# Kernel tuning notes

Measured on AMD Instinct MI355X. Metric: run time of the kernel, lower is better.

Reference implementation:

```python
import jax, jax.numpy as jnp
import numpy as np


def setup_inputs() -> dict:
    key = jax.random.key(0)
    B, N, D = 8, 2048, 512
    put = jax.random.normal(key, (B, N, D), dtype=jnp.float32)
    return {"put": put, "k": 16}


def reference(put, k):
    # put: [B, N, D]; k: python int
    B, N, _ = put.shape
    # squared-norm expansion of pairwise Euclidean distance
    xx = jnp.sum(put * put, axis=2, keepdims=True)            # [B, N, 1]
    gram = jnp.einsum('bnd,bmd->bnm', put, put)               # [B, N, N]
    dist2 = xx + jnp.swapaxes(xx, 1, 2) - 2.0 * gram          # [B, N, N]
    dist = jnp.sqrt(jnp.clip(dist2, 0.0))                     # clamp(min=0).sqrt()

    # k nearest (smallest distance): top_k of negated distances
    _, inc = jax.lax.top_k(-dist, k)                          # [B, N, k] int32

    # binary adjacency: out[b, j, inc[b, j, :]] = 1 (vectorized scatter)
    b_idx = jnp.arange(B)[:, None, None]                      # [B,1,1]
    r_idx = jnp.arange(N)[None, :, None]                      # [1,N,1]
    out = jnp.zeros_like(dist).at[b_idx, r_idx, inc].set(1.0)
    return out
```

## Files before the change

kernel.cpp:

```cpp
#include <hip/hip_runtime.h>
#include <cstdint>

#define NN 2048
#define DD 512
#define NB 8

using ull = unsigned long long;
typedef __attribute__((ext_vector_type(8))) short bf16x8;
typedef __attribute__((ext_vector_type(4))) float f32x4;

#define GLOAD_LDS16(g, l)                                                      \
  __builtin_amdgcn_global_load_lds(                                            \
      (const __attribute__((address_space(1))) unsigned int*)(g),              \
      (__attribute__((address_space(3))) unsigned int*)(l), 16, 0, 0)

__device__ inline unsigned short f2bf(float f) {
  unsigned u = __float_as_uint(f);
  unsigned r = u + 0x7FFFu + ((u >> 16) & 1u);
  return (unsigned short)(r >> 16);
}

__global__ __launch_bounds__(256) void knn_prep(const float* __restrict__ put,
                                                float* __restrict__ norms32,
                                                unsigned short* __restrict__ bhalf) {
  const int row  = blockIdx.x * 4 + (threadIdx.x >> 6);
  const int lane = threadIdx.x & 63;
  const float* p = put + (size_t)row * DD + lane * 8;
  float4 x0 = ((const float4*)p)[0];
  float4 x1 = ((const float4*)p)[1];
  double s = (double)x0.x * (double)x0.x + (double)x0.y * (double)x0.y +
             (double)x0.z * (double)x0.z + (double)x0.w * (double)x0.w +
             (double)x1.x * (double)x1.x + (double)x1.y * (double)x1.y +
             (double)x1.z * (double)x1.z + (double)x1.w * (double)x1.w;
  uint4 v;
  v.x = (unsigned)f2bf(x0.x) | ((unsigned)f2bf(x0.y) << 16);
  v.y = (unsigned)f2bf(x0.z) | ((unsigned)f2bf(x0.w) << 16);
  v.z = (unsigned)f2bf(x1.x) | ((unsigned)f2bf(x1.y) << 16);
  v.w = (unsigned)f2bf(x1.z) | ((unsigned)f2bf(x1.w) << 16);
  *((uint4*)(bhalf + (size_t)row * DD) + lane) = v;
#pragma unroll
  for (int m = 1; m < 64; m <<= 1) s += __shfl_xor(s, m, 64);
  if (lane == 0) norms32[row] = (float)s;
}

__global__ __launch_bounds__(256) void knn_gemm(
    const unsigned short* __restrict__ bhalf,
    const float* __restrict__ norms32,
    unsigned short* __restrict__ Sws) {
  __shared__ unsigned short smem[16384];
  unsigned short* As = smem;
  unsigned short* Bs = smem + 4096;

  const int t    = threadIdx.x;
  const int lane = t & 63;
  const int wv   = t >> 6;
  const int q    = lane >> 4;
  const int l15  = lane & 15;
  const int wrow = wv >> 1, wcol = wv & 1;
  const int m0 = blockIdx.x * 128;
  const int j0 = blockIdx.y * 128;
  const int b  = blockIdx.z;

  const unsigned short* pb = bhalf + (size_t)b * NN * DD;

  const int rloc = lane >> 2;
  const int kcg  = (lane & 3) ^ ((lane >> 3) & 3);
  const int i0 = 2 * wv, i1 = 2 * wv + 1;
  const unsigned short* gA0 = pb + (size_t)(j0 + 16 * i0 + rloc) * DD + kcg * 8;
  const unsigned short* gA1 = pb + (size_t)(j0 + 16 * i1 + rloc) * DD + kcg * 8;
  const unsigned short* gB0 = pb + (size_t)(m0 + 16 * i0 + rloc) * DD + kcg * 8;
  const unsigned short* gB1 = pb + (size_t)(m0 + 16 * i1 + rloc) * DD + kcg * 8;
  unsigned short* lA0 = As + i0 * 512;
  unsigned short* lA1 = As + i1 * 512;
  unsigned short* lB0 = Bs + i0 * 512;
  unsigned short* lB1 = Bs + i1 * 512;

  const int xsw = (q ^ ((l15 >> 1) & 3)) * 8;

  f32x4 acc[4][4];
  const f32x4 zz = {0.f, 0.f, 0.f, 0.f};
#pragma unroll
  for (int i = 0; i < 4; ++i)
#pragma unroll
    for (int j = 0; j < 4; ++j) acc[i][j] = zz;

  for (int kt = 0; kt < DD; kt += 32) {
    __syncthreads();
    GLOAD_LDS16(gA0, lA0);
    GLOAD_LDS16(gA1, lA1);
    GLOAD_LDS16(gB0, lB0);
    GLOAD_LDS16(gB1, lB1);
    gA0 += 32; gA1 += 32; gB0 += 32; gB1 += 32;
    __syncthreads();

    bf16x8 af[4], bg[4];
#pragma unroll
    for (int f = 0; f < 4; ++f) {
      af[f] = *(const bf16x8*)(As + (wrow * 64 + f * 16 + l15) * 32 + xsw);
      bg[f] = *(const bf16x8*)(Bs + (wcol * 64 + f * 16 + l15) * 32 + xsw);
    }
#pragma unroll
    for (int fi = 0; fi < 4; ++fi)
#pragma unroll
      for (int fj = 0; fj < 4; ++fj)
        acc[fi][fj] = __builtin_amdgcn_mfma_f32_16x16x32_bf16(
            af[fi], bg[fj], acc[fi][fj], 0, 0, 0);
  }

  float xn[4];
#pragma unroll
  for (int fj = 0; fj < 4; ++fj)
    xn[fj] = norms32[(size_t)b * NN + m0 + wcol * 64 + fj * 16 + l15];

  __syncthreads();
  unsigned short* Sl = smem + wv * 4096;
#pragma unroll
  for (int fi = 0; fi < 4; ++fi)
#pragma unroll
    for (int fj = 0; fj < 4; ++fj)
#pragma unroll
      for (int r = 0; r < 4; ++r) {
        float sv = xn[fj] - 2.0f * acc[fi][fj][r] + 2048.0f;
        Sl[(fi * 16 + q * 4 + r) * 64 + fj * 16 + l15] =
            __builtin_bit_cast(unsigned short, (_Float16)sv);
      }

  const size_t row0 = (size_t)(b * NN + j0 + wrow * 64);
#pragma unroll
  for (int it = 0; it < 8; ++it) {
    int idx = it * 64 + lane;
    int row = idx >> 3, c8 = idx & 7;
    uint4 v = *(const uint4*)(Sl + row * 64 + c8 * 8);
    *(uint4*)(Sws + (row0 + row) * NN + m0 + wcol * 64 + c8 * 8) = v;
  }
}

__device__ inline void ins8(unsigned (&h)[8], unsigned k) {
#pragma unroll
  for (int p = 0; p < 8; ++p) {
    unsigned lo = min(h[p], k);
    k = max(h[p], k);
    h[p] = lo;
  }
}

__global__ __launch_bounds__(256) void knn_select(
    const unsigned short* __restrict__ Sws,
    const float* __restrict__ put,
    const float* __restrict__ norms32,
    float* __restrict__ out) {
  __shared__ unsigned candL[4][32];
  __shared__ double part[4][32][9];
  __shared__ ull keyL[4][32];
  __shared__ unsigned winL[4][16];

  const int wv   = threadIdx.x >> 6;
  const int lane = threadIdx.x & 63;
  const int R = blockIdx.x * 4 + wv;
  const int b = R >> 11, j = R & (NN - 1);

  unsigned h[8];
#pragma unroll
  for (int p = 0; p < 8; ++p) h[p] = 0xFFFFFFFFu;
  const unsigned short* Srow = Sws + (size_t)R * NN;
#pragma unroll
  for (int i = 0; i < 4; ++i) {
    uint4 u = *(const uint4*)(Srow + i * 512 + lane * 8);
    unsigned base = (unsigned)(i * 512 + lane * 8);
    ins8(h, (u.x << 16) | base);
    ins8(h, (u.x & 0xFFFF0000u) | (base + 1));
    ins8(h, (u.y << 16) | (base + 2));
    ins8(h, (u.y & 0xFFFF0000u) | (base + 3));
    ins8(h, (u.z << 16) | (base + 4));
    ins8(h, (u.z & 0xFFFF0000u) | (base + 5));
    ins8(h, (u.w << 16) | (base + 6));
    ins8(h, (u.w & 0xFFFF0000u) | (base + 7));
  }

  for (int r = 0; r < 32; ++r) {
    unsigned w = h[0];
#pragma unroll
    for (int m = 1; m < 64; m <<= 1)
      w = min(w, (unsigned)__shfl_xor((int)w, m, 64));
    if (h[0] == w) {
      candL[wv][r] = w & 0xFFFFu;
#pragma unroll
      for (int p = 0; p < 7; ++p) h[p] = h[p + 1];
      h[7] = 0xFFFFFFFFu;
    }
  }

  const float* panel = put + (size_t)b * NN * DD;
  const float* xjp = panel + (size_t)j * DD + lane * 8;
  float4 xa = ((const float4*)xjp)[0];
  float4 xb = ((const float4*)xjp)[1];
  double x0 = xa.x, x1 = xa.y, x2 = xa.z, x3 = xa.w;
  double x4 = xb.x, x5 = xb.y, x6 = xb.z, x7 = xb.w;

  for (int c = 0; c < 32; ++c) {
    int cand = (int)candL[wv][c];
    const float* cr = panel + (size_t)cand * DD + lane * 8;
    float4 ya = ((const float4*)cr)[0];
    float4 yb = ((const float4*)cr)[1];
    double p = x0 * (double)ya.x + x1 * (double)ya.y + x2 * (double)ya.z +
               x3 * (double)ya.w + x4 * (double)yb.x + x5 * (double)yb.y +
               x6 * (double)yb.z + x7 * (double)yb.w;
    p += __shfl_xor(p, 1, 64);
    p += __shfl_xor(p, 2, 64);
    p += __shfl_xor(p, 4, 64);
    if ((lane & 7) == 0) part[wv][c][lane >> 3] = p;
  }

  if (lane < 32) {
    double dot = part[wv][lane][0] + part[wv][lane][1] + part[wv][lane][2] +
                 part[wv][lane][3] + part[wv][lane][4] + part[wv][lane][5] +
                 part[wv][lane][6] + part[wv][lane][7];
    int cand = (int)candL[wv][lane];
    float g32 = (float)dot;
    float xxm = norms32[(size_t)b * NN + cand];
    float xxj = norms32[(size_t)b * NN + j];
    float s   = __fadd_rn(xxj, xxm);
    float d2  = __fsub_rn(s, __fmul_rn(2.0f, g32));
    d2 = fmaxf(d2, 0.0f);
    float dist = __fsqrt_rn(d2);
    keyL[wv][lane] = ((ull)__float_as_uint(dist) << 32) | (unsigned)cand;
  }
  if (lane < 32) {
    ull mine = keyL[wv][lane];
    int rank = 0;
#pragma unroll
    for (int i = 0; i < 32; ++i) rank += (keyL[wv][i] < mine) ? 1 : 0;
    if (rank < 16) winL[wv][rank] = (unsigned)(keyL[wv][lane] & 0xFFFFULL);
  }

  unsigned mask = 0;
#pragma unroll
  for (int i = 0; i < 16; ++i) {
    unsigned c = winL[wv][i];
    unsigned own = (((c >> 2) & 63u) == (unsigned)lane) ? 1u : 0u;
    unsigned bit = (((c >> 8) & 7u) << 2) | (c & 3u);
    mask |= own << bit;
  }
  float* orow = out + (size_t)R * NN;
#pragma unroll
  for (int it = 0; it < 8; ++it) {
    float4 v;
    v.x = (float)((mask >> (it * 4 + 0)) & 1u);
    v.y = (float)((mask >> (it * 4 + 1)) & 1u);
    v.z = (float)((mask >> (it * 4 + 2)) & 1u);
    v.w = (float)((mask >> (it * 4 + 3)) & 1u);
    ((float4*)(orow + it * 256))[lane] = v;
  }
}

extern "C" void kernel_launch(void* const* d_in, const int* in_sizes, int n_in,
                              void* d_out, int out_size, void* d_ws, size_t ws_size,
                              hipStream_t stream) {
  const float* put = (const float*)d_in[0];
  float* out = (float*)d_out;

  float* norms32 = (float*)d_ws;
  unsigned short* bhalf = (unsigned short*)((char*)d_ws + 65536);
  unsigned short* Sws =
      (unsigned short*)((char*)d_ws + 65536 + (size_t)NB * NN * DD * 2);

  knn_prep<<<dim3(NB * NN / 4), 256, 0, stream>>>(put, norms32, bhalf);
  knn_gemm<<<dim3(16, 16, 8), 256, 0, stream>>>(bhalf, norms32, Sws);
  knn_select<<<dim3(NB * NN / 4), 256, 0, stream>>>(Sws, put, norms32, out);
}
```

Before: 294.8 us.

## Exploit Gram symmetry in GEMM, shrink candidate set, batch fp64 rescoring loads

The GEMM now computes only upper-triangular 128x128 tiles (136 per batch) and writes each off-diagonal tile twice, once transposed via a padded shared-memory staging buffer with per-row norms. This cuts the MFMA work roughly in half at the cost of extra stores and a serial tile-index decode. The select kernel also keeps 24 fp16-screened candidates instead of 32 before exact fp64 rescoring, and unrolls the rescoring loop 4-wide so more global loads are in flight. Fewer candidates raises the risk of missing a true neighbour when fp16/bf16 errors reorder close distances.

```diff
diff --git a/kernel.cpp b/kernel.cpp
--- a/kernel.cpp
+++ b/kernel.cpp
@@ -4,6 +4,7 @@
 #define NN 2048
 #define DD 512
 #define NB 8
+#define NCAND 24
 
 using ull = unsigned long long;
 typedef __attribute__((ext_vector_type(8))) short bf16x8;
@@ -47,9 +48,14 @@
     const unsigned short* __restrict__ bhalf,
     const float* __restrict__ norms32,
     unsigned short* __restrict__ Sws) {
-  __shared__ unsigned short smem[16384];
+  __shared__ unsigned short smem[18432];
   unsigned short* As = smem;
   unsigned short* Bs = smem + 4096;
+
+  int idx = blockIdx.x;
+  int jt = 0;
+  while (idx >= 16 - jt) { idx -= 16 - jt; ++jt; }
+  const int mt = jt + idx;
 
   const int t    = threadIdx.x;
   const int lane = t & 63;
@@ -57,9 +63,9 @@
   const int q    = lane >> 4;
   const int l15  = lane & 15;
   const int wrow = wv >> 1, wcol = wv & 1;
-  const int m0 = blockIdx.x * 128;
-  const int j0 = blockIdx.y * 128;
-  const int b  = blockIdx.z;
+  const int m0 = mt * 128;
+  const int j0 = jt * 128;
+  const int b  = blockIdx.y;
 
   const unsigned short* pb = bhalf + (size_t)b * NN * DD;
 
@@ -128,10 +134,41 @@
   const size_t row0 = (size_t)(b * NN + j0 + wrow * 64);
 #pragma unroll
   for (int it = 0; it < 8; ++it) {
-    int idx = it * 64 + lane;
-    int row = idx >> 3, c8 = idx & 7;
+    int i2 = it * 64 + lane;
+    int row = i2 >> 3, c8 = i2 & 7;
     uint4 v = *(const uint4*)(Sl + row * 64 + c8 * 8);
     *(uint4*)(Sws + (row0 + row) * NN + m0 + wcol * 64 + c8 * 8) = v;
+  }
+
+  if (jt != mt) {
+    float xr[16];
+#pragma unroll
+    for (int fi = 0; fi < 4; ++fi)
+#pragma unroll
+      for (int r = 0; r < 4; ++r)
+        xr[fi * 4 + r] =
+            norms32[(size_t)b * NN + j0 + wrow * 64 + fi * 16 + q * 4 + r];
+
+    __syncthreads();
+    unsigned short* Mw = smem + wv * 4608;
+#pragma unroll
+    for (int fi = 0; fi < 4; ++fi)
+#pragma unroll
+      for (int fj = 0; fj < 4; ++fj)
+#pragma unroll
+        for (int r = 0; r < 4; ++r) {
+          float sv = xr[fi * 4 + r] - 2.0f * acc[fi][fj][r] + 2048.0f;
+          Mw[(fj * 16 + l15) * 72 + fi * 16 + q * 4 + r] =
+              __builtin_bit_cast(unsigned short, (_Float16)sv);
+        }
+    const size_t mrow0 = (size_t)(b * NN + m0 + wcol * 64);
+#pragma unroll
+    for (int it = 0; it < 8; ++it) {
+      int i2 = it * 64 + lane;
+      int row = i2 >> 3, c8 = i2 & 7;
+      uint4 v = *(const uint4*)(Mw + row * 72 + c8 * 8);
+      *(uint4*)(Sws + (mrow0 + row) * NN + j0 + wrow * 64 + c8 * 8) = v;
+    }
   }
 }
 
@@ -149,9 +186,9 @@
     const float* __restrict__ put,
     const float* __restrict__ norms32,
     float* __restrict__ out) {
-  __shared__ unsigned candL[4][32];
-  __shared__ double part[4][32][9];
-  __shared__ ull keyL[4][32];
+  __shared__ unsigned candL[4][NCAND];
+  __shared__ double part[4][NCAND][9];
+  __shared__ ull keyL[4][NCAND];
   __shared__ unsigned winL[4][16];
 
   const int wv   = threadIdx.x >> 6;
@@ -177,7 +214,7 @@
     ins8(h, (u.w & 0xFFFF0000u) | (base + 7));
   }
 
-  for (int r = 0; r < 32; ++r) {
+  for (int r = 0; r < NCAND; ++r) {
     unsigned w = h[0];
 #pragma unroll
     for (int m = 1; m < 64; m <<= 1)
@@ -197,21 +234,28 @@
   double x0 = xa.x, x1 = xa.y, x2 = xa.z, x3 = xa.w;
   double x4 = xb.x, x5 = xb.y, x6 = xb.z, x7 = xb.w;
 
-  for (int c = 0; c < 32; ++c) {
-    int cand = (int)candL[wv][c];
-    const float* cr = panel + (size_t)cand * DD + lane * 8;
-    float4 ya = ((const float4*)cr)[0];
-    float4 yb = ((const float4*)cr)[1];
-    double p = x0 * (double)ya.x + x1 * (double)ya.y + x2 * (double)ya.z +
-               x3 * (double)ya.w + x4 * (double)yb.x + x5 * (double)yb.y +
-               x6 * (double)yb.z + x7 * (double)yb.w;
-    p += __shfl_xor(p, 1, 64);
-    p += __shfl_xor(p, 2, 64);
-    p += __shfl_xor(p, 4, 64);
-    if ((lane & 7) == 0) part[wv][c][lane >> 3] = p;
-  }
-
-  if (lane < 32) {
+  for (int c0 = 0; c0 < NCAND; c0 += 4) {
+    double p[4];
+#pragma unroll
+    for (int u = 0; u < 4; ++u) {
+      int cand = (int)candL[wv][c0 + u];
+      const float4* cr = (const float4*)(panel + (size_t)cand * DD + lane * 8);
+      float4 ya = cr[0];
+      float4 yb = cr[1];
+      p[u] = x0 * (double)ya.x + x1 * (double)ya.y + x2 * (double)ya.z +
+             x3 * (double)ya.w + x4 * (double)yb.x + x5 * (double)yb.y +
+             x6 * (double)yb.z + x7 * (double)yb.w;
+    }
+#pragma unroll
+    for (int u = 0; u < 4; ++u) {
+      p[u] += __shfl_xor(p[u], 1, 64);
+      p[u] += __shfl_xor(p[u], 2, 64);
+      p[u] += __shfl_xor(p[u], 4, 64);
+      if ((lane & 7) == 0) part[wv][c0 + u][lane >> 3] = p[u];
+    }
+  }
+
+  if (lane < NCAND) {
     double dot = part[wv][lane][0] + part[wv][lane][1] + part[wv][lane][2] +
                  part[wv][lane][3] + part[wv][lane][4] + part[wv][lane][5] +
                  part[wv][lane][6] + part[wv][lane][7];
@@ -225,11 +269,11 @@
     float dist = __fsqrt_rn(d2);
     keyL[wv][lane] = ((ull)__float_as_uint(dist) << 32) | (unsigned)cand;
   }
-  if (lane < 32) {
+  if (lane < NCAND) {
     ull mine = keyL[wv][lane];
     int rank = 0;
 #pragma unroll
-    for (int i = 0; i < 32; ++i) rank += (keyL[wv][i] < mine) ? 1 : 0;
+    for (int i = 0; i < NCAND; ++i) rank += (keyL[wv][i] < mine) ? 1 : 0;
     if (rank < 16) winL[wv][rank] = (unsigned)(keyL[wv][lane] & 0xFFFFULL);
   }
 
@@ -265,6 +309,6 @@
       (unsigned short*)((char*)d_ws + 65536 + (size_t)NB * NN * DD * 2);
 
   knn_prep<<<dim3(NB * NN / 4), 256, 0, stream>>>(put, norms32, bhalf);
-  knn_gemm<<<dim3(16, 16, 8), 256, 0, stream>>>(bhalf, norms32, Sws);
+  knn_gemm<<<dim3(136, NB), 256, 0, stream>>>(bhalf, norms32, Sws);
   knn_select<<<dim3(NB * NN / 4), 256, 0, stream>>>(Sws, put, norms32, out);
 }
```

Result: faster. 253.0 us (-14.2%).
